# Optimization experiments

Measured on AMD Instinct MI355X. Metric: run time of the kernel, lower is better.

Reference implementation:

```python
import jax, jax.numpy as jnp
import numpy as np

B, T, H = 32, 2048, 1024

def setup_inputs() -> dict:
    key = jax.random.key(0)
    k1, k2, k3 = jax.random.split(key, 3)
    hidden = jax.random.normal(k1, (B, H), dtype=jnp.float32)
    encoder_outputs = jax.random.normal(k2, (B, T, H), dtype=jnp.float32)
    W = jax.random.normal(k3, (H, H), dtype=jnp.float32) / np.sqrt(H)
    return {"hidden": hidden, "encoder_outputs": encoder_outputs, "W": W}

def reference(hidden, encoder_outputs, W):
    # Linear (no bias): torch nn.Linear applies x @ W.T
    encoder_transformed = jnp.einsum('bth,oh->bto', encoder_outputs, W)
    # score: [B, T] = bmm([B,T,H], [B,H,1]).squeeze
    score = jnp.einsum('bth,bh->bt', encoder_transformed, hidden)
    attention_weights = jax.nn.softmax(score, axis=1)
    # context: [B, H]
    context_vector = jnp.einsum('bt,bth->bh', attention_weights, encoder_outputs)
    return (context_vector, attention_weights)
```

## Files before the change

### kernel.cpp

```cpp
#include <hip/hip_runtime.h>

#define B 32
#define T 2048
#define H 1024

__global__ __launch_bounds__(256) void compute_v_kernel(
    const float* __restrict__ hidden, const float* __restrict__ W,
    float* __restrict__ v) {
  __shared__ float sh[H];
  const int b = blockIdx.y;
  const int h = blockIdx.x * 256 + threadIdx.x;
  for (int i = threadIdx.x; i < H; i += 256) sh[i] = hidden[b * H + i];
  __syncthreads();
  float acc = 0.f;
#pragma unroll 8
  for (int o = 0; o < H; ++o) acc = fmaf(sh[o], W[o * H + h], acc);
  v[b * H + h] = acc;
}

__global__ __launch_bounds__(256) void scores_kernel(
    const float* __restrict__ enc, const float* __restrict__ v,
    float* __restrict__ score) {
  const int b = blockIdx.y;
  const int wave = threadIdx.x >> 6;
  const int lane = threadIdx.x & 63;
  const float4* v4 = (const float4*)(v + b * H);
  float4 vr[4];
#pragma unroll
  for (int j = 0; j < 4; ++j) vr[j] = v4[j * 64 + lane];
  const int t0 = blockIdx.x * 128;
  for (int it = 0; it < 32; ++it) {
    const int t = t0 + it * 4 + wave;
    const float4* e4 = (const float4*)(enc + ((size_t)b * T + t) * H);
    float acc = 0.f;
#pragma unroll
    for (int j = 0; j < 4; ++j) {
      float4 e = e4[j * 64 + lane];
      acc += e.x * vr[j].x + e.y * vr[j].y + e.z * vr[j].z + e.w * vr[j].w;
    }
#pragma unroll
    for (int off = 32; off; off >>= 1) acc += __shfl_down(acc, off, 64);
    if (lane == 0) score[b * T + t] = acc;
  }
}

__global__ __launch_bounds__(256) void softmax_kernel(float* __restrict__ score) {
  const int b = blockIdx.x;
  const int tid = threadIdx.x;
  const int wave = tid >> 6;
  const int lane = tid & 63;
  __shared__ float red[4];
  float* row = score + b * T;

  float x[8];
  float m = -1e30f;
#pragma unroll
  for (int j = 0; j < 8; ++j) {
    x[j] = row[j * 256 + tid];
    m = fmaxf(m, x[j]);
  }
#pragma unroll
  for (int off = 32; off; off >>= 1) m = fmaxf(m, __shfl_down(m, off, 64));
  if (lane == 0) red[wave] = m;
  __syncthreads();
  m = fmaxf(fmaxf(red[0], red[1]), fmaxf(red[2], red[3]));
  __syncthreads();

  float e[8];
  float s = 0.f;
#pragma unroll
  for (int j = 0; j < 8; ++j) {
    e[j] = __expf(x[j] - m);
    s += e[j];
  }
#pragma unroll
  for (int off = 32; off; off >>= 1) s += __shfl_down(s, off, 64);
  if (lane == 0) red[wave] = s;
  __syncthreads();
  const float inv = 1.f / (red[0] + red[1] + red[2] + red[3]);
#pragma unroll
  for (int j = 0; j < 8; ++j) row[j * 256 + tid] = e[j] * inv;
}

#define TCH 128
#define NCH (T / TCH)
__global__ __launch_bounds__(256) void context_partial_kernel(
    const float* __restrict__ enc, const float* __restrict__ attn,
    float* __restrict__ partial) {
  const int b = blockIdx.y;
  const int c = blockIdx.x;
  const int tid = threadIdx.x;
  __shared__ float wa[TCH];
  if (tid < TCH) wa[tid] = attn[b * T + c * TCH + tid];
  __syncthreads();
  float4 acc = {0.f, 0.f, 0.f, 0.f};
  const float4* base = (const float4*)(enc + ((size_t)b * T + c * TCH) * H);
  for (int t = 0; t < TCH; ++t) {
    const float w = wa[t];
    float4 e = base[(size_t)t * (H / 4) + tid];
    acc.x = fmaf(w, e.x, acc.x);
    acc.y = fmaf(w, e.y, acc.y);
    acc.z = fmaf(w, e.z, acc.z);
    acc.w = fmaf(w, e.w, acc.w);
  }
  ((float4*)(partial + ((size_t)b * NCH + c) * H))[tid] = acc;
}

__global__ __launch_bounds__(256) void context_reduce_kernel(
    const float* __restrict__ partial, float* __restrict__ ctx) {
  const int b = blockIdx.x;
  const int tid = threadIdx.x;
  float4 acc = {0.f, 0.f, 0.f, 0.f};
  const float4* p = (const float4*)(partial + (size_t)b * NCH * H);
#pragma unroll
  for (int c = 0; c < NCH; ++c) {
    float4 e = p[c * (H / 4) + tid];
    acc.x += e.x;
    acc.y += e.y;
    acc.z += e.z;
    acc.w += e.w;
  }
  ((float4*)(ctx + b * H))[tid] = acc;
}

extern "C" void kernel_launch(void* const* d_in, const int* in_sizes, int n_in,
                              void* d_out, int out_size, void* d_ws,
                              size_t ws_size, hipStream_t stream) {
  const float* hidden = (const float*)d_in[0];
  const float* enc = (const float*)d_in[1];
  const float* W = (const float*)d_in[2];

  float* out = (float*)d_out;
  float* out_ctx = out;
  float* out_attn = out + B * H;

  float* v = (float*)d_ws;
  float* partial = v + B * H;

  compute_v_kernel<<<dim3(H / 256, B), 256, 0, stream>>>(hidden, W, v);
  scores_kernel<<<dim3(T / 128, B), 256, 0, stream>>>(enc, v, out_attn);
  softmax_kernel<<<B, 256, 0, stream>>>(out_attn);
  context_partial_kernel<<<dim3(NCH, B), 256, 0, stream>>>(enc, out_attn, partial);
  context_reduce_kernel<<<B, 256, 0, stream>>>(partial, out_ctx);
}
```

Baseline: 470.3 us.

## Split-K compute_v, pair rows in scores, fuse softmax normalization into context pass

New measurement: 424.5 us. -9.7%, faster.

```diff
diff --git a/kernel.cpp b/kernel.cpp
--- a/kernel.cpp
+++ b/kernel.cpp
@@ -7,15 +7,29 @@
 __global__ __launch_bounds__(256) void compute_v_kernel(
     const float* __restrict__ hidden, const float* __restrict__ W,
     float* __restrict__ v) {
+  const int b = blockIdx.y;
+  const int og = threadIdx.x >> 6;
+  const int hl = threadIdx.x & 63;
+  const int h = blockIdx.x * 64 + hl;
   __shared__ float sh[H];
-  const int b = blockIdx.y;
-  const int h = blockIdx.x * 256 + threadIdx.x;
+  __shared__ float red[4][64];
   for (int i = threadIdx.x; i < H; i += 256) sh[i] = hidden[b * H + i];
   __syncthreads();
-  float acc = 0.f;
-#pragma unroll 8
-  for (int o = 0; o < H; ++o) acc = fmaf(sh[o], W[o * H + h], acc);
-  v[b * H + h] = acc;
+  float acc[8] = {0.f, 0.f, 0.f, 0.f, 0.f, 0.f, 0.f, 0.f};
+  const int ob = og * 256;
+  for (int oo = 0; oo < 256; oo += 8) {
+#pragma unroll
+    for (int k = 0; k < 8; ++k) {
+      const int o = ob + oo + k;
+      acc[k] = fmaf(sh[o], W[(size_t)o * H + h], acc[k]);
+    }
+  }
+  float a = ((acc[0] + acc[1]) + (acc[2] + acc[3])) +
+            ((acc[4] + acc[5]) + (acc[6] + acc[7]));
+  red[og][hl] = a;
+  __syncthreads();
+  if (og == 0)
+    v[b * H + h] = (red[0][hl] + red[1][hl]) + (red[2][hl] + red[3][hl]);
 }
 
 __global__ __launch_bounds__(256) void scores_kernel(
@@ -28,29 +42,44 @@
   float4 vr[4];
 #pragma unroll
   for (int j = 0; j < 4; ++j) vr[j] = v4[j * 64 + lane];
-  const int t0 = blockIdx.x * 128;
-  for (int it = 0; it < 32; ++it) {
-    const int t = t0 + it * 4 + wave;
-    const float4* e4 = (const float4*)(enc + ((size_t)b * T + t) * H);
-    float acc = 0.f;
+  const int t0 = blockIdx.x * 64 + wave * 16;
+  for (int it = 0; it < 16; it += 2) {
+    const int ta = t0 + it, tb = t0 + it + 1;
+    const float4* ea4 = (const float4*)(enc + ((size_t)b * T + ta) * H);
+    const float4* eb4 = (const float4*)(enc + ((size_t)b * T + tb) * H);
+    float4 ea[4], eb[4];
+#pragma unroll
+    for (int j = 0; j < 4; ++j) ea[j] = ea4[j * 64 + lane];
+#pragma unroll
+    for (int j = 0; j < 4; ++j) eb[j] = eb4[j * 64 + lane];
+    float accA = 0.f, accB = 0.f;
 #pragma unroll
     for (int j = 0; j < 4; ++j) {
-      float4 e = e4[j * 64 + lane];
-      acc += e.x * vr[j].x + e.y * vr[j].y + e.z * vr[j].z + e.w * vr[j].w;
+      accA += ea[j].x * vr[j].x + ea[j].y * vr[j].y + ea[j].z * vr[j].z +
+              ea[j].w * vr[j].w;
+      accB += eb[j].x * vr[j].x + eb[j].y * vr[j].y + eb[j].z * vr[j].z +
+              eb[j].w * vr[j].w;
     }
 #pragma unroll
-    for (int off = 32; off; off >>= 1) acc += __shfl_down(acc, off, 64);
-    if (lane == 0) score[b * T + t] = acc;
+    for (int off = 32; off; off >>= 1) {
+      accA += __shfl_down(accA, off, 64);
+      accB += __shfl_down(accB, off, 64);
+    }
+    if (lane == 0) {
+      score[b * T + ta] = accA;
+      score[b * T + tb] = accB;
+    }
   }
 }
 
-__global__ __launch_bounds__(256) void softmax_kernel(float* __restrict__ score) {
+__global__ __launch_bounds__(256) void softmax_stats_kernel(
+    const float* __restrict__ score, float2* __restrict__ stats) {
   const int b = blockIdx.x;
   const int tid = threadIdx.x;
   const int wave = tid >> 6;
   const int lane = tid & 63;
   __shared__ float red[4];
-  float* row = score + b * T;
+  const float* row = score + b * T;
 
   float x[8];
   float m = -1e30f;
@@ -66,59 +95,72 @@
   m = fmaxf(fmaxf(red[0], red[1]), fmaxf(red[2], red[3]));
   __syncthreads();
 
-  float e[8];
   float s = 0.f;
 #pragma unroll
-  for (int j = 0; j < 8; ++j) {
-    e[j] = __expf(x[j] - m);
-    s += e[j];
-  }
+  for (int j = 0; j < 8; ++j) s += __expf(x[j] - m);
 #pragma unroll
   for (int off = 32; off; off >>= 1) s += __shfl_down(s, off, 64);
   if (lane == 0) red[wave] = s;
   __syncthreads();
-  const float inv = 1.f / (red[0] + red[1] + red[2] + red[3]);
-#pragma unroll
-  for (int j = 0; j < 8; ++j) row[j * 256 + tid] = e[j] * inv;
+  if (tid == 0) {
+    const float total = (red[0] + red[1]) + (red[2] + red[3]);
+    stats[b] = make_float2(m, 1.f / total);
+  }
 }
 
-#define TCH 128
+#define TCH 64
 #define NCH (T / TCH)
 __global__ __launch_bounds__(256) void context_partial_kernel(
-    const float* __restrict__ enc, const float* __restrict__ attn,
-    float* __restrict__ partial) {
+    const float* __restrict__ enc, float* __restrict__ attn,
+    const float2* __restrict__ stats, float* __restrict__ partial) {
   const int b = blockIdx.y;
   const int c = blockIdx.x;
   const int tid = threadIdx.x;
   __shared__ float wa[TCH];
-  if (tid < TCH) wa[tid] = attn[b * T + c * TCH + tid];
+  const float2 st = stats[b];
+  if (tid < TCH) {
+    const float raw = attn[b * T + c * TCH + tid];
+    const float w = __expf(raw - st.x) * st.y;
+    attn[b * T + c * TCH + tid] = w;
+    wa[tid] = w;
+  }
   __syncthreads();
-  float4 acc = {0.f, 0.f, 0.f, 0.f};
+  float4 a0 = {0, 0, 0, 0}, a1 = {0, 0, 0, 0}, a2 = {0, 0, 0, 0},
+         a3 = {0, 0, 0, 0};
   const float4* base = (const float4*)(enc + ((size_t)b * T + c * TCH) * H);
-  for (int t = 0; t < TCH; ++t) {
-    const float w = wa[t];
-    float4 e = base[(size_t)t * (H / 4) + tid];
-    acc.x = fmaf(w, e.x, acc.x);
-    acc.y = fmaf(w, e.y, acc.y);
-    acc.z = fmaf(w, e.z, acc.z);
-    acc.w = fmaf(w, e.w, acc.w);
+  for (int t = 0; t < TCH; t += 4) {
+    float4 e0 = base[(size_t)(t + 0) * (H / 4) + tid];
+    float4 e1 = base[(size_t)(t + 1) * (H / 4) + tid];
+    float4 e2 = base[(size_t)(t + 2) * (H / 4) + tid];
+    float4 e3 = base[(size_t)(t + 3) * (H / 4) + tid];
+    const float w0 = wa[t], w1 = wa[t + 1], w2 = wa[t + 2], w3 = wa[t + 3];
+    a0.x = fmaf(w0, e0.x, a0.x); a0.y = fmaf(w0, e0.y, a0.y);
+    a0.z = fmaf(w0, e0.z, a0.z); a0.w = fmaf(w0, e0.w, a0.w);
+    a1.x = fmaf(w1, e1.x, a1.x); a1.y = fmaf(w1, e1.y, a1.y);
+    a1.z = fmaf(w1, e1.z, a1.z); a1.w = fmaf(w1, e1.w, a1.w);
+    a2.x = fmaf(w2, e2.x, a2.x); a2.y = fmaf(w2, e2.y, a2.y);
+    a2.z = fmaf(w2, e2.z, a2.z); a2.w = fmaf(w2, e2.w, a2.w);
+    a3.x = fmaf(w3, e3.x, a3.x); a3.y = fmaf(w3, e3.y, a3.y);
+    a3.z = fmaf(w3, e3.z, a3.z); a3.w = fmaf(w3, e3.w, a3.w);
   }
-  ((float4*)(partial + ((size_t)b * NCH + c) * H))[tid] = acc;
+  float4 r;
+  r.x = (a0.x + a1.x) + (a2.x + a3.x);
+  r.y = (a0.y + a1.y) + (a2.y + a3.y);
+  r.z = (a0.z + a1.z) + (a2.z + a3.z);
+  r.w = (a0.w + a1.w) + (a2.w + a3.w);
+  ((float4*)(partial + ((size_t)b * NCH + c) * H))[tid] = r;
 }
 
 __global__ __launch_bounds__(256) void context_reduce_kernel(
     const float* __restrict__ partial, float* __restrict__ ctx) {
   const int b = blockIdx.x;
   const int tid = threadIdx.x;
-  float4 acc = {0.f, 0.f, 0.f, 0.f};
+  float4 acc = {0, 0, 0, 0};
   const float4* p = (const float4*)(partial + (size_t)b * NCH * H);
-#pragma unroll
+#pragma unroll 8
   for (int c = 0; c < NCH; ++c) {
     float4 e = p[c * (H / 4) + tid];
-    acc.x += e.x;
-    acc.y += e.y;
-    acc.z += e.z;
-    acc.w += e.w;
+    acc.x += e.x; acc.y += e.y; acc.z += e.z; acc.w += e.w;
   }
   ((float4*)(ctx + b * H))[tid] = acc;
 }
@@ -136,10 +178,12 @@
 
   float* v = (float*)d_ws;
   float* partial = v + B * H;
+  float2* stats = (float2*)(partial + B * NCH * H);
 
-  compute_v_kernel<<<dim3(H / 256, B), 256, 0, stream>>>(hidden, W, v);
-  scores_kernel<<<dim3(T / 128, B), 256, 0, stream>>>(enc, v, out_attn);
-  softmax_kernel<<<B, 256, 0, stream>>>(out_attn);
-  context_partial_kernel<<<dim3(NCH, B), 256, 0, stream>>>(enc, out_attn, partial);
+  compute_v_kernel<<<dim3(H / 64, B), 256, 0, stream>>>(hidden, W, v);
+  scores_kernel<<<dim3(T / 64, B), 256, 0, stream>>>(enc, v, out_attn);
+  softmax_stats_kernel<<<B, 256, 0, stream>>>(out_attn, stats);
+  context_partial_kernel<<<dim3(NCH, B), 256, 0, stream>>>(enc, out_attn, stats,
+                                                           partial);
   context_reduce_kernel<<<B, 256, 0, stream>>>(partial, out_ctx);
 }
```
